# Kernel optimization log

Hardware: AMD Instinct MI355X
Metric: run time of the kernel (lower is better)

Reference implementation:

```python
import jax, jax.numpy as jnp
import numpy as np
from jax import lax

N, C_IN, C_OUT, H, W = 8, 64, 64, 128, 128
K, KS, STRIDE, PAD, GROUPS = 4, 3, 1, 1, 1


def setup_inputs() -> dict:
    key = jax.random.key(0)
    ks = jax.random.split(key, 10)
    s = 0.05
    return {
        "x": jax.random.normal(ks[0], (N, C_IN, H, W), jnp.float32),
        "weight": jax.random.normal(ks[1], (K, C_OUT, C_IN // GROUPS, KS, KS), jnp.float32) * s,
        "conv_w": jax.random.normal(ks[2], (C_OUT, C_IN, KS, KS), jnp.float32) * s,
        "conv_b": jax.random.normal(ks[3], (C_OUT,), jnp.float32) * s,
        "net0_w": jax.random.normal(ks[4], (K, 1, 1, 1, 1), jnp.float32) * s,
        "net0_b": jax.random.normal(ks[5], (K,), jnp.float32) * s,
        "net1_w": jax.random.normal(ks[6], (K, 1, 3, 3, 3), jnp.float32) * s,
        "net1_b": jax.random.normal(ks[7], (K,), jnp.float32) * s,
        "net2_w": jax.random.normal(ks[8], (K, 1, 5, 3, 3), jnp.float32) * s,
        "net2_b": jax.random.normal(ks[9], (K,), jnp.float32) * s,
    }


def _conv3d_mean(x5, w, b, pad):
    # x5: (N,1,C,H,W); w: (K,1,kd,kh,kw); 'same'-style padding per kernel.
    y = lax.conv_general_dilated(x5, w, (1, 1, 1), [(p, p) for p in pad],
                                 dimension_numbers=('NCDHW', 'OIDHW', 'NCDHW'))
    # global avg pool over (C,H,W); bias is constant so add after the mean.
    return jnp.mean(y, axis=(2, 3, 4)) + b[None, :]


def reference(x, weight, conv_w, conv_b, net0_w, net0_b, net1_w, net1_b, net2_w, net2_b):
    dn2 = ('NCHW', 'OIHW', 'NCHW')
    # static residual conv branch
    r = lax.conv_general_dilated(x, conv_w, (STRIDE, STRIDE), [(PAD, PAD)] * 2,
                                 dimension_numbers=dn2) + conv_b[None, :, None, None]
    # attention over 3D convs of x.unsqueeze(1)
    x5 = x[:, None]  # (N,1,C,H,W)
    logits = (_conv3d_mean(x5, net0_w, net0_b, (0, 0, 0))
              + _conv3d_mean(x5, net1_w, net1_b, (1, 1, 1))
              + _conv3d_mean(x5, net2_w, net2_b, (2, 1, 1)))  # (N,K)
    att = jax.nn.softmax(logits, axis=-1)
    # per-sample dynamic kernel mixing: (N,K) @ (K,out,in/g,kh,kw)
    agg_w = jnp.einsum('nk,koihw->noihw', att, weight)
    # grouped conv with groups = GROUPS*N == per-sample conv (vmapped)
    def per_sample(xi, wi):
        return lax.conv_general_dilated(xi[None], wi, (STRIDE, STRIDE), [(PAD, PAD)] * 2,
                                        dimension_numbers=dn2,
                                        feature_group_count=GROUPS)[0]
    out = jax.vmap(per_sample)(x, agg_w)  # (N,out,H,W)
    return out + r
```

## Files before the change

kernel.cpp:

```cpp
#include <hip/hip_runtime.h>


typedef unsigned short ushort_t;
typedef __attribute__((ext_vector_type(8))) short bf16x8;
typedef __attribute__((ext_vector_type(4))) float f32x4;

__device__ __forceinline__ ushort_t f2bf(float f) {
    unsigned u = __float_as_uint(f);
    unsigned r = (u + 0x7fffu + ((u >> 16) & 1u)) >> 16;
    return (ushort_t)r;
}

__global__ __launch_bounds__(256) void kT(const float* __restrict__ x,
                                          ushort_t* __restrict__ xt) {
    int g = blockIdx.x * 256 + threadIdx.x;
    int w   = g & 127;
    int rest = g >> 7;
    int cig = rest & 7;
    int nh  = rest >> 3;
    int h   = nh & 127;
    int n   = nh >> 7;

    const float* xp = x + (((size_t)(n * 64) * 128 + h) * 128 + w);
    ushort_t vals[8];
#pragma unroll
    for (int j = 0; j < 8; ++j) {
        int ci = cig * 8 + j;
        vals[j] = f2bf(xp[(size_t)ci * (128 * 128)]);
    }
    uint4 v;
    v.x = (unsigned)vals[0] | ((unsigned)vals[1] << 16);
    v.y = (unsigned)vals[2] | ((unsigned)vals[3] << 16);
    v.z = (unsigned)vals[4] | ((unsigned)vals[5] << 16);
    v.w = (unsigned)vals[6] | ((unsigned)vals[7] << 16);
    *(uint4*)(xt + ((size_t)nh * 128 + w) * 64 + cig * 8) = v;
}

__global__ __launch_bounds__(128) void kR(const float* __restrict__ x,
                                          float* __restrict__ cat) {
    int bid = blockIdx.x;
    int n = bid >> 6, d = bid & 63;
    int w = threadIdx.x;
    const float* xp = x + ((size_t)(n * 64 + d) * 128) * 128 + w;
    float a0 = 0.f, a1 = 0.f, a2 = 0.f;
#pragma unroll 4
    for (int h = 0; h < 128; ++h) {
        float v = xp[h * 128];
        if (h == 0) a0 += v;
        else if (h == 127) a2 += v;
        else a1 += v;
    }
    __shared__ float s[128][3];
    s[w][0] = a0; s[w][1] = a1; s[w][2] = a2;
    __syncthreads();
    if (threadIdx.x < 9) {
        int ch = threadIdx.x / 3, st = threadIdx.x % 3;
        float v;
        if (st == 0) { v = 0.f; for (int i = 0; i < 128; ++i) v += s[i][ch]; }
        else if (st == 1) v = s[0][ch];
        else v = s[127][ch];
        int cd = (d == 0) ? 0 : (d == 1) ? 1 : (d == 62) ? 3 : (d == 63) ? 4 : 2;
        atomicAdd(&cat[((n * 5 + cd) * 3 + ch) * 3 + st], v);
    }
}

__global__ void kA(const float* __restrict__ cat,
                   const float* __restrict__ nw0, const float* __restrict__ nb0,
                   const float* __restrict__ nw1, const float* __restrict__ nb1,
                   const float* __restrict__ nw2, const float* __restrict__ nb2,
                   float* __restrict__ att) {
    int t = threadIdx.x;
    int n = t >> 2, k = t & 3;

    float c[5][3][3];
#pragma unroll
    for (int i = 0; i < 5; ++i)
#pragma unroll
        for (int j = 0; j < 3; ++j)
#pragma unroll
            for (int s = 0; s < 3; ++s)
                c[i][j][s] = cat[((n * 5 + i) * 3 + j) * 3 + s];

    const float invV = 1.0f / (64.f * 128.f * 128.f);

    auto box = [&](int sd, int sh, int sw) -> float {
        float acc = 0.f;
#pragma unroll
        for (int cd = 0; cd < 5; ++cd) {
            int dv = (cd == 0) ? 0 : (cd == 1) ? 1 : (cd == 3) ? 62 : (cd == 4) ? 63 : -1;
            bool incd = (dv < 0) || (dv >= sd && dv < 64 + sd);
#pragma unroll
            for (int ch = 0; ch < 3; ++ch) {
                int hv = (ch == 0) ? 0 : (ch == 2) ? 127 : -1;
                bool inch = (hv < 0) || (hv >= sh && hv < 128 + sh);
                if (incd && inch) {
                    float v = c[cd][ch][0];
                    if (sw == -1) v -= c[cd][ch][2];
                    else if (sw == 1) v -= c[cd][ch][1];
                    acc += v;
                }
            }
        }
        return acc;
    };

    float lg = nb0[k] + nb1[k] + nb2[k];
    {
        float tot = 0.f;
#pragma unroll
        for (int i = 0; i < 5; ++i)
#pragma unroll
            for (int j = 0; j < 3; ++j) tot += c[i][j][0];
        lg += nw0[k] * tot * invV;
    }
#pragma unroll
    for (int dz = 0; dz < 3; ++dz)
#pragma unroll
        for (int dy = 0; dy < 3; ++dy)
#pragma unroll
            for (int dx = 0; dx < 3; ++dx)
                lg += nw1[k * 27 + dz * 9 + dy * 3 + dx] *
                      box(dz - 1, dy - 1, dx - 1) * invV;
#pragma unroll
    for (int dz = 0; dz < 5; ++dz)
#pragma unroll
        for (int dy = 0; dy < 3; ++dy)
#pragma unroll
            for (int dx = 0; dx < 3; ++dx)
                lg += nw2[k * 45 + dz * 9 + dy * 3 + dx] *
                      box(dz - 2, dy - 1, dx - 1) * invV;

    float m = fmaxf(lg, __shfl_xor(lg, 1));
    m = fmaxf(m, __shfl_xor(m, 2));
    float e = __expf(lg - m);
    float ssum = e + __shfl_xor(e, 1);
    ssum += __shfl_xor(ssum, 2);
    att[t] = e / ssum;
}

__global__ __launch_bounds__(256) void kW(const float* __restrict__ att,
                                          const float* __restrict__ weight,
                                          const float* __restrict__ convw,
                                          ushort_t* __restrict__ weff) {
    int g = blockIdx.x * 256 + threadIdx.x;
    int ci = g & 63;
    int co = (g >> 6) & 63;
    int rest = g >> 12;
    int s = rest % 9;
    int n = rest / 9;
    float v = convw[(co * 64 + ci) * 9 + s];
#pragma unroll
    for (int k = 0; k < 4; ++k)
        v += att[n * 4 + k] * weight[((k * 64 + co) * 64 + ci) * 9 + s];
    weff[g] = f2bf(v);
}

__global__ __launch_bounds__(256) void kC(const ushort_t* __restrict__ xt,
                                          const ushort_t* __restrict__ weff,
                                          const float* __restrict__ convb,
                                          float* __restrict__ out) {
    int bid = blockIdx.x;
    int wt = bid & 1;
    int h = (bid >> 1) & 127;
    int n = bid >> 8;
    int w0 = wt * 64;

    __shared__ __align__(16) ushort_t lds[3 * 66 * 72];

    int tid = threadIdx.x;
    int lane = tid & 63;
    int wave = tid >> 6;
    int kq = lane >> 4;
    int l15 = lane & 15;

    for (int idx = tid; idx < 1584; idx += 256) {
        int ci8 = idx & 7;
        int rc = idx >> 3;
        int c = rc % 66;
        int r = rc / 66;
        int hg = h + r - 1;
        int wg = w0 + c - 1;
        uint4 v = make_uint4(0u, 0u, 0u, 0u);
        if (hg >= 0 && hg < 128 && wg >= 0 && wg < 128) {
            v = *(const uint4*)(xt + (((size_t)n * 128 + hg) * 128 + wg) * 64 + ci8 * 8);
        }
        *(uint4*)&lds[(r * 66 + c) * 72 + ci8 * 8] = v;
    }

    int co_a = wave * 16 + l15;
    bf16x8 afrag[9][2];
#pragma unroll
    for (int s = 0; s < 9; ++s)
#pragma unroll
        for (int kc = 0; kc < 2; ++kc)
            afrag[s][kc] = *(const bf16x8*)(weff +
                ((size_t)((n * 9 + s) * 64 + co_a)) * 64 + kc * 32 + kq * 8);

    f32x4 acc[4];
#pragma unroll
    for (int nt = 0; nt < 4; ++nt) acc[nt] = (f32x4){0.f, 0.f, 0.f, 0.f};

    __syncthreads();

#pragma unroll
    for (int s = 0; s < 9; ++s) {
        int ky = s / 3, kx = s % 3;
#pragma unroll
        for (int kc = 0; kc < 2; ++kc) {
#pragma unroll
            for (int nt = 0; nt < 4; ++nt) {
                int sp = nt * 16 + l15;
                bf16x8 bfrag = *(const bf16x8*)&lds[(ky * 66 + sp + kx) * 72 + kc * 32 + kq * 8];
                acc[nt] = __builtin_amdgcn_mfma_f32_16x16x32_bf16(
                    afrag[s][kc], bfrag, acc[nt], 0, 0, 0);
            }
        }
    }

#pragma unroll
    for (int nt = 0; nt < 4; ++nt) {
#pragma unroll
        for (int reg = 0; reg < 4; ++reg) {
            int co = wave * 16 + kq * 4 + reg;
            int sp = w0 + nt * 16 + l15;
            float v = acc[nt][reg] + convb[co];
            out[(((size_t)n * 64 + co) * 128 + h) * 128 + sp] = v;
        }
    }
}

extern "C" void kernel_launch(void* const* d_in, const int* in_sizes, int n_in,
                              void* d_out, int out_size, void* d_ws, size_t ws_size,
                              hipStream_t stream) {
    const float* x      = (const float*)d_in[0];
    const float* weight = (const float*)d_in[1];
    const float* conv_w = (const float*)d_in[2];
    const float* conv_b = (const float*)d_in[3];
    const float* n0w    = (const float*)d_in[4];
    const float* n0b    = (const float*)d_in[5];
    const float* n1w    = (const float*)d_in[6];
    const float* n1b    = (const float*)d_in[7];
    const float* n2w    = (const float*)d_in[8];
    const float* n2b    = (const float*)d_in[9];
    float* out = (float*)d_out;

    char* ws = (char*)d_ws;
    ushort_t* xt   = (ushort_t*)(ws);
    ushort_t* weff = (ushort_t*)(ws + 16777216);
    float*    cat  = (float*)(ws + 16777216 + 589824);
    float*    att  = (float*)(ws + 16777216 + 589824 + 1440);

    hipMemsetAsync(cat, 0, 1440, stream);
    kT<<<4096, 256, 0, stream>>>(x, xt);
    kR<<<512, 128, 0, stream>>>(x, cat);
    kA<<<1, 32, 0, stream>>>(cat, n0w, n0b, n1w, n1b, n2w, n2b, att);
    kW<<<1152, 256, 0, stream>>>(att, weight, conv_w, weff);
    kC<<<2048, 256, 0, stream>>>(xt, weff, conv_b, out);
}
```

Measured before the change: 153.5 us.

## Fuse transpose with reduction, fold attention into weight mixing, two rows per conv block

Merges the bf16 channel-last transpose and the boundary-sum reduction into one kernel that reads x once, staging through LDS and using warp shuffles plus local atomics. The attention softmax moves inside the weight-mixing kernel, so three launches become three kernels instead of five. The conv kernel now computes two output rows per block, reusing the halo rows and the A fragments across more MFMAs. The cost is fewer blocks, higher register pressure, and a weight-mixing kernel with only 32 blocks that is partly serialized on the softmax.

```diff
diff --git a/kernel.cpp b/kernel.cpp
--- a/kernel.cpp
+++ b/kernel.cpp
@@ -11,148 +11,157 @@
     return (ushort_t)r;
 }
 
-__global__ __launch_bounds__(256) void kT(const float* __restrict__ x,
-                                          ushort_t* __restrict__ xt) {
-    int g = blockIdx.x * 256 + threadIdx.x;
-    int w   = g & 127;
-    int rest = g >> 7;
-    int cig = rest & 7;
-    int nh  = rest >> 3;
-    int h   = nh & 127;
-    int n   = nh >> 7;
-
-    const float* xp = x + (((size_t)(n * 64) * 128 + h) * 128 + w);
-    ushort_t vals[8];
-#pragma unroll
-    for (int j = 0; j < 8; ++j) {
-        int ci = cig * 8 + j;
-        vals[j] = f2bf(xp[(size_t)ci * (128 * 128)]);
-    }
-    uint4 v;
-    v.x = (unsigned)vals[0] | ((unsigned)vals[1] << 16);
-    v.y = (unsigned)vals[2] | ((unsigned)vals[3] << 16);
-    v.z = (unsigned)vals[4] | ((unsigned)vals[5] << 16);
-    v.w = (unsigned)vals[6] | ((unsigned)vals[7] << 16);
-    *(uint4*)(xt + ((size_t)nh * 128 + w) * 64 + cig * 8) = v;
-}
-
-__global__ __launch_bounds__(128) void kR(const float* __restrict__ x,
-                                          float* __restrict__ cat) {
+__global__ __launch_bounds__(256) void kTR(const float* __restrict__ x,
+                                           ushort_t* __restrict__ xt,
+                                           float* __restrict__ cat) {
     int bid = blockIdx.x;
-    int n = bid >> 6, d = bid & 63;
-    int w = threadIdx.x;
-    const float* xp = x + ((size_t)(n * 64 + d) * 128) * 128 + w;
-    float a0 = 0.f, a1 = 0.f, a2 = 0.f;
-#pragma unroll 4
-    for (int h = 0; h < 128; ++h) {
-        float v = xp[h * 128];
-        if (h == 0) a0 += v;
-        else if (h == 127) a2 += v;
-        else a1 += v;
-    }
-    __shared__ float s[128][3];
-    s[w][0] = a0; s[w][1] = a1; s[w][2] = a2;
-    __syncthreads();
-    if (threadIdx.x < 9) {
-        int ch = threadIdx.x / 3, st = threadIdx.x % 3;
-        float v;
-        if (st == 0) { v = 0.f; for (int i = 0; i < 128; ++i) v += s[i][ch]; }
-        else if (st == 1) v = s[0][ch];
-        else v = s[127][ch];
-        int cd = (d == 0) ? 0 : (d == 1) ? 1 : (d == 62) ? 3 : (d == 63) ? 4 : 2;
-        atomicAdd(&cat[((n * 5 + cd) * 3 + ch) * 3 + st], v);
-    }
-}
-
-__global__ void kA(const float* __restrict__ cat,
-                   const float* __restrict__ nw0, const float* __restrict__ nb0,
-                   const float* __restrict__ nw1, const float* __restrict__ nb1,
-                   const float* __restrict__ nw2, const float* __restrict__ nb2,
-                   float* __restrict__ att) {
-    int t = threadIdx.x;
-    int n = t >> 2, k = t & 3;
-
-    float c[5][3][3];
-#pragma unroll
-    for (int i = 0; i < 5; ++i)
-#pragma unroll
-        for (int j = 0; j < 3; ++j)
-#pragma unroll
-            for (int s = 0; s < 3; ++s)
-                c[i][j][s] = cat[((n * 5 + i) * 3 + j) * 3 + s];
-
-    const float invV = 1.0f / (64.f * 128.f * 128.f);
-
-    auto box = [&](int sd, int sh, int sw) -> float {
-        float acc = 0.f;
-#pragma unroll
-        for (int cd = 0; cd < 5; ++cd) {
-            int dv = (cd == 0) ? 0 : (cd == 1) ? 1 : (cd == 3) ? 62 : (cd == 4) ? 63 : -1;
-            bool incd = (dv < 0) || (dv >= sd && dv < 64 + sd);
-#pragma unroll
-            for (int ch = 0; ch < 3; ++ch) {
-                int hv = (ch == 0) ? 0 : (ch == 2) ? 127 : -1;
-                bool inch = (hv < 0) || (hv >= sh && hv < 128 + sh);
-                if (incd && inch) {
-                    float v = c[cd][ch][0];
-                    if (sw == -1) v -= c[cd][ch][2];
-                    else if (sw == 1) v -= c[cd][ch][1];
-                    acc += v;
-                }
-            }
-        }
-        return acc;
-    };
-
-    float lg = nb0[k] + nb1[k] + nb2[k];
-    {
-        float tot = 0.f;
-#pragma unroll
-        for (int i = 0; i < 5; ++i)
-#pragma unroll
-            for (int j = 0; j < 3; ++j) tot += c[i][j][0];
-        lg += nw0[k] * tot * invV;
-    }
-#pragma unroll
-    for (int dz = 0; dz < 3; ++dz)
-#pragma unroll
-        for (int dy = 0; dy < 3; ++dy)
-#pragma unroll
-            for (int dx = 0; dx < 3; ++dx)
-                lg += nw1[k * 27 + dz * 9 + dy * 3 + dx] *
-                      box(dz - 1, dy - 1, dx - 1) * invV;
-#pragma unroll
-    for (int dz = 0; dz < 5; ++dz)
-#pragma unroll
-        for (int dy = 0; dy < 3; ++dy)
-#pragma unroll
-            for (int dx = 0; dx < 3; ++dx)
-                lg += nw2[k * 45 + dz * 9 + dy * 3 + dx] *
-                      box(dz - 2, dy - 1, dx - 1) * invV;
-
-    float m = fmaxf(lg, __shfl_xor(lg, 1));
-    m = fmaxf(m, __shfl_xor(m, 2));
-    float e = __expf(lg - m);
-    float ssum = e + __shfl_xor(e, 1);
-    ssum += __shfl_xor(ssum, 2);
-    att[t] = e / ssum;
-}
-
-__global__ __launch_bounds__(256) void kW(const float* __restrict__ att,
+    int h = bid & 127, n = bid >> 7;
+    int tid = threadIdx.x;
+
+    __shared__ ushort_t t[128 * 72];
+    __shared__ float catloc[15];
+    if (tid < 15) catloc[tid] = 0.f;
+    __syncthreads();
+
+    const float* xp = x + (size_t)n * 64 * 16384 + h * 128;
+    int wq = tid & 31;
+
+#pragma unroll
+    for (int i = 0; i < 8; ++i) {
+        int idx = i * 256 + tid;
+        int ci = idx >> 5;
+        float4 v = *(const float4*)(xp + (size_t)ci * 16384 + wq * 4);
+
+        int w0 = wq * 4;
+        t[(w0 + 0) * 72 + ci] = f2bf(v.x);
+        t[(w0 + 1) * 72 + ci] = f2bf(v.y);
+        t[(w0 + 2) * 72 + ci] = f2bf(v.z);
+        t[(w0 + 3) * 72 + ci] = f2bf(v.w);
+
+        float s4 = v.x + v.y + v.z + v.w;
+#pragma unroll
+        for (int m = 1; m <= 16; m <<= 1) s4 += __shfl_xor(s4, m);
+        int cd = (ci == 0) ? 0 : (ci == 1) ? 1 : (ci == 62) ? 3 : (ci == 63) ? 4 : 2;
+        if (wq == 0) {
+            atomicAdd(&catloc[cd * 3 + 0], s4);
+            atomicAdd(&catloc[cd * 3 + 1], v.x);
+        }
+        if (wq == 31) atomicAdd(&catloc[cd * 3 + 2], v.w);
+    }
+    __syncthreads();
+
+    ushort_t* op = xt + ((size_t)(n * 128 + h)) * 128 * 64;
+#pragma unroll
+    for (int j = 0; j < 4; ++j) {
+        int q = j * 256 + tid;
+        int w = q >> 3, ci8 = q & 7;
+        uint4 v = *(const uint4*)&t[w * 72 + ci8 * 8];
+        *(uint4*)(op + (size_t)w * 64 + ci8 * 8) = v;
+    }
+
+    if (tid < 15) {
+        int cd = tid / 3, st = tid % 3;
+        int ch = (h == 0) ? 0 : (h == 127) ? 2 : 1;
+        atomicAdd(&cat[((n * 5 + cd) * 3 + ch) * 3 + st], catloc[tid]);
+    }
+}
+
+__global__ __launch_bounds__(256) void kW(const float* __restrict__ cat,
+                                          const float* __restrict__ nw0, const float* __restrict__ nb0,
+                                          const float* __restrict__ nw1, const float* __restrict__ nb1,
+                                          const float* __restrict__ nw2, const float* __restrict__ nb2,
                                           const float* __restrict__ weight,
                                           const float* __restrict__ convw,
                                           ushort_t* __restrict__ weff) {
-    int g = blockIdx.x * 256 + threadIdx.x;
-    int ci = g & 63;
-    int co = (g >> 6) & 63;
-    int rest = g >> 12;
-    int s = rest % 9;
-    int n = rest / 9;
-    float v = convw[(co * 64 + ci) * 9 + s];
-#pragma unroll
-    for (int k = 0; k < 4; ++k)
-        v += att[n * 4 + k] * weight[((k * 64 + co) * 64 + ci) * 9 + s];
-    weff[g] = f2bf(v);
+    int n = blockIdx.x >> 2, q = blockIdx.x & 3;
+    int tid = threadIdx.x;
+    __shared__ float att_s[4];
+
+    if (tid < 4) {
+        int k = tid;
+        float c[5][3][3];
+#pragma unroll
+        for (int i = 0; i < 5; ++i)
+#pragma unroll
+            for (int j = 0; j < 3; ++j)
+#pragma unroll
+                for (int s = 0; s < 3; ++s)
+                    c[i][j][s] = cat[((n * 5 + i) * 3 + j) * 3 + s];
+
+        const float invV = 1.0f / (64.f * 128.f * 128.f);
+        auto box = [&](int sd, int sh, int sw) -> float {
+            float acc = 0.f;
+#pragma unroll
+            for (int cd = 0; cd < 5; ++cd) {
+                int dv = (cd == 0) ? 0 : (cd == 1) ? 1 : (cd == 3) ? 62 : (cd == 4) ? 63 : -1;
+                bool incd = (dv < 0) || (dv >= sd && dv < 64 + sd);
+#pragma unroll
+                for (int ch = 0; ch < 3; ++ch) {
+                    int hv = (ch == 0) ? 0 : (ch == 2) ? 127 : -1;
+                    bool inch = (hv < 0) || (hv >= sh && hv < 128 + sh);
+                    if (incd && inch) {
+                        float v = c[cd][ch][0];
+                        if (sw == -1) v -= c[cd][ch][2];
+                        else if (sw == 1) v -= c[cd][ch][1];
+                        acc += v;
+                    }
+                }
+            }
+            return acc;
+        };
+
+        float lg = nb0[k] + nb1[k] + nb2[k];
+        {
+            float tot = 0.f;
+#pragma unroll
+            for (int i = 0; i < 5; ++i)
+#pragma unroll
+                for (int j = 0; j < 3; ++j) tot += c[i][j][0];
+            lg += nw0[k] * tot * invV;
+        }
+#pragma unroll
+        for (int dz = 0; dz < 3; ++dz)
+#pragma unroll
+            for (int dy = 0; dy < 3; ++dy)
+#pragma unroll
+                for (int dx = 0; dx < 3; ++dx)
+                    lg += nw1[k * 27 + dz * 9 + dy * 3 + dx] *
+                          box(dz - 1, dy - 1, dx - 1) * invV;
+#pragma unroll
+        for (int dz = 0; dz < 5; ++dz)
+#pragma unroll
+            for (int dy = 0; dy < 3; ++dy)
+#pragma unroll
+                for (int dx = 0; dx < 3; ++dx)
+                    lg += nw2[k * 45 + dz * 9 + dy * 3 + dx] *
+                          box(dz - 2, dy - 1, dx - 1) * invV;
+
+        float m = fmaxf(lg, __shfl_xor(lg, 1));
+        m = fmaxf(m, __shfl_xor(m, 2));
+        float e = __expf(lg - m);
+        float ssum = e + __shfl_xor(e, 1);
+        ssum += __shfl_xor(ssum, 2);
+        att_s[k] = e / ssum;
+    }
+    __syncthreads();
+
+    float a0 = att_s[0], a1 = att_s[1], a2 = att_s[2], a3 = att_s[3];
+    int ci = tid & 63;
+    int co_base = q * 16 + (tid >> 6) * 4;
+#pragma unroll
+    for (int p = 0; p < 4; ++p) {
+        int co = co_base + p;
+        const float* cw = convw + (size_t)(co * 64 + ci) * 9;
+        const float* w0 = weight + (size_t)((0 * 64 + co) * 64 + ci) * 9;
+        const float* w1 = weight + (size_t)((1 * 64 + co) * 64 + ci) * 9;
+        const float* w2 = weight + (size_t)((2 * 64 + co) * 64 + ci) * 9;
+        const float* w3 = weight + (size_t)((3 * 64 + co) * 64 + ci) * 9;
+#pragma unroll
+        for (int s = 0; s < 9; ++s) {
+            float v = cw[s] + a0 * w0[s] + a1 * w1[s] + a2 * w2[s] + a3 * w3[s];
+            weff[((size_t)(n * 9 + s) * 64 + co) * 64 + ci] = f2bf(v);
+        }
+    }
 }
 
 __global__ __launch_bounds__(256) void kC(const ushort_t* __restrict__ xt,
@@ -161,11 +170,12 @@
                                           float* __restrict__ out) {
     int bid = blockIdx.x;
     int wt = bid & 1;
-    int h = (bid >> 1) & 127;
-    int n = bid >> 8;
+    int hp = (bid >> 1) & 63;
+    int n = bid >> 7;
+    int h0 = hp * 2;
     int w0 = wt * 64;
 
-    __shared__ __align__(16) ushort_t lds[3 * 66 * 72];
+    __shared__ __align__(16) ushort_t lds[4 * 66 * 72];
 
     int tid = threadIdx.x;
     int lane = tid & 63;
@@ -173,12 +183,12 @@
     int kq = lane >> 4;
     int l15 = lane & 15;
 
-    for (int idx = tid; idx < 1584; idx += 256) {
+    for (int idx = tid; idx < 2112; idx += 256) {
         int ci8 = idx & 7;
         int rc = idx >> 3;
         int c = rc % 66;
         int r = rc / 66;
-        int hg = h + r - 1;
+        int hg = h0 + r - 1;
         int wg = w0 + c - 1;
         uint4 v = make_uint4(0u, 0u, 0u, 0u);
         if (hg >= 0 && hg < 128 && wg >= 0 && wg < 128) {
@@ -196,9 +206,9 @@
             afrag[s][kc] = *(const bf16x8*)(weff +
                 ((size_t)((n * 9 + s) * 64 + co_a)) * 64 + kc * 32 + kq * 8);
 
-    f32x4 acc[4];
-#pragma unroll
-    for (int nt = 0; nt < 4; ++nt) acc[nt] = (f32x4){0.f, 0.f, 0.f, 0.f};
+    f32x4 acc[8];
+#pragma unroll
+    for (int nt = 0; nt < 8; ++nt) acc[nt] = (f32x4){0.f, 0.f, 0.f, 0.f};
 
     __syncthreads();
 
@@ -208,9 +218,11 @@
 #pragma unroll
         for (int kc = 0; kc < 2; ++kc) {
 #pragma unroll
-            for (int nt = 0; nt < 4; ++nt) {
-                int sp = nt * 16 + l15;
-                bf16x8 bfrag = *(const bf16x8*)&lds[(ky * 66 + sp + kx) * 72 + kc * 32 + kq * 8];
+            for (int nt = 0; nt < 8; ++nt) {
+                int r = nt >> 2;
+                int wl = (nt & 3) * 16 + l15;
+                bf16x8 bfrag = *(const bf16x8*)
+                    &lds[((r + ky) * 66 + wl + kx) * 72 + kc * 32 + kq * 8];
                 acc[nt] = __builtin_amdgcn_mfma_f32_16x16x32_bf16(
                     afrag[s][kc], bfrag, acc[nt], 0, 0, 0);
             }
@@ -218,13 +230,14 @@
     }
 
 #pragma unroll
-    for (int nt = 0; nt < 4; ++nt) {
+    for (int nt = 0; nt < 8; ++nt) {
+        int h = h0 + (nt >> 2);
+        int w = w0 + (nt & 3) * 16 + l15;
 #pragma unroll
         for (int reg = 0; reg < 4; ++reg) {
             int co = wave * 16 + kq * 4 + reg;
-            int sp = w0 + nt * 16 + l15;
             float v = acc[nt][reg] + convb[co];
-            out[(((size_t)n * 64 + co) * 128 + h) * 128 + sp] = v;
+            out[(((size_t)n * 64 + co) * 128 + h) * 128 + w] = v;
         }
     }
 }
@@ -248,12 +261,10 @@
     ushort_t* xt   = (ushort_t*)(ws);
     ushort_t* weff = (ushort_t*)(ws + 16777216);
     float*    cat  = (float*)(ws + 16777216 + 589824);
-    float*    att  = (float*)(ws + 16777216 + 589824 + 1440);
 
     hipMemsetAsync(cat, 0, 1440, stream);
-    kT<<<4096, 256, 0, stream>>>(x, xt);
-    kR<<<512, 128, 0, stream>>>(x, cat);
-    kA<<<1, 32, 0, stream>>>(cat, n0w, n0b, n1w, n1b, n2w, n2b, att);
-    kW<<<1152, 256, 0, stream>>>(att, weight, conv_w, weff);
-    kC<<<2048, 256, 0, stream>>>(xt, weff, conv_b, out);
-}
+    kTR<<<1024, 256, 0, stream>>>(x, xt, cat);
+    kW<<<32, 256, 0, stream>>>(cat, n0w, n0b, n1w, n1b, n2w, n2b,
+                               weight, conv_w, weff);
+    kC<<<1024, 256, 0, stream>>>(xt, weff, conv_b, out);
+}
```

Result: faster. 143.2 us (-6.7%).
